# Kernel optimization log

Hardware: AMD Instinct MI355X
Metric: run time of the kernel (lower is better)

## Reference

```python
import jax, jax.numpy as jnp
import numpy as np

NEG_BIG = -1e12
ALPHA = 0.2  # LeakyReLU negative slope

def setup_inputs() -> dict:
    key = jax.random.key(0)
    k1, k2, k3, k4, k5 = jax.random.split(key, 5)
    N, F_in, F_out = 8192, 256, 128
    inp = jax.random.normal(k1, (N, F_in), dtype=jnp.float32)
    adj = jax.random.randint(k2, (N, N), 0, 2, dtype=jnp.int32)
    W = jax.random.normal(k3, (F_in, F_out), dtype=jnp.float32) * 0.05
    W_2 = jax.random.normal(k4, (F_in, F_out), dtype=jnp.float32) * 0.05
    W_3 = jax.random.normal(k5, (F_in, F_out), dtype=jnp.float32) * 0.05
    return {"inp": inp, "adj": adj, "W": W, "W_2": W_2, "W_3": W_3}

def reference(inp, adj, W, W_2, W_3):
    # h = inp @ W, h_2 = inp @ W_2  -> scores e = LeakyReLU(h @ h_2^T)  [N, N]
    h = inp @ W
    h_2 = inp @ W_2
    e = jax.nn.leaky_relu(h @ h_2.T, negative_slope=ALPHA)
    # adjacency mask, row softmax (dropout disabled: eval mode)
    attention = jax.nn.softmax(jnp.where(adj > 0, e, NEG_BIG), axis=1)
    h_3 = inp @ W_3
    h_prime = attention @ h_3
    return jax.nn.elu(h_prime)  # concat=True path
```

## Files before the change

### kernel.cpp

```cpp
#include <hip/hip_runtime.h>
#include <hip/hip_fp16.h>

#define N    8192
#define FIN  256
#define FOUT 128
#define BM   64
#define BN   64

typedef _Float16 half8 __attribute__((ext_vector_type(8)));
typedef _Float16 half4v __attribute__((ext_vector_type(4)));
typedef float floatx4 __attribute__((ext_vector_type(4)));

__global__ __launch_bounds__(256)
void maskprep_kernel(const int* __restrict__ adj,
                     unsigned long long* __restrict__ Msk)
{
    const int tid  = threadIdx.x;
    const int wave = tid >> 6;
    const int lane = tid & 63;
    const int task = blockIdx.x * 4 + wave;
    const int row  = task >> 3;
    const int g0   = (task & 7) * 4;
    const int4* base = (const int4*)(adj + (size_t)row * N);
    int4 v[4];
#pragma unroll
    for (int gg = 0; gg < 4; gg++) v[gg] = base[(g0 + gg) * 64 + lane];
#pragma unroll
    for (int gg = 0; gg < 4; gg++) {
        unsigned long long b0 = __ballot(v[gg].x != 0);
        unsigned long long b1 = __ballot(v[gg].y != 0);
        unsigned long long b2 = __ballot(v[gg].z != 0);
        unsigned long long b3 = __ballot(v[gg].w != 0);
        if (lane == 0) {
            unsigned long long* p = &Msk[((size_t)row * 32 + g0 + gg) * 4];
            *(ulonglong2*)&p[0] = make_ulonglong2(b0, b1);
            *(ulonglong2*)&p[2] = make_ulonglong2(b2, b3);
        }
    }
}

__global__ __launch_bounds__(256)
void wprep_kernel(const float* __restrict__ W0,
                  const float* __restrict__ W1,
                  const float* __restrict__ W2,
                  _Float16* __restrict__ Wf)
{
    int idx  = blockIdx.x * 256 + threadIdx.x;
    int lane = idx & 63;
    int frag = idx >> 6;
    int w    = frag >> 6;
    int f    = frag & 63;
    int nt   = f >> 3, kc = f & 7;
    int quad = lane >> 4, lo16 = lane & 15;
    const float* Wp = w == 0 ? W0 : (w == 1 ? W1 : W2);
    half8 v;
#pragma unroll
    for (int jj = 0; jj < 8; jj++)
        v[jj] = (_Float16)Wp[(size_t)(kc * 32 + quad * 8 + jj) * FOUT + nt * 16 + lo16];
    *(half8*)&Wf[(size_t)idx * 8] = v;
}

__global__ __launch_bounds__(256, 2)
void gemm3_kernel(const float* __restrict__ inp,
                  const _Float16* __restrict__ Wf,
                  _Float16* __restrict__ H,
                  _Float16* __restrict__ H2,
                  _Float16* __restrict__ H3T)
{
    const int which = blockIdx.z;
    const int c0    = blockIdx.y * 64;
    const _Float16* Wfw = Wf + (size_t)which * 64 * 64 * 8;
    const int r0 = blockIdx.x * 64;
    const int tid  = threadIdx.x;
    const int wave = tid >> 6;
    const int lane = tid & 63;
    const int lo16 = lane & 15;
    const int quad = lane >> 4;
    const int r = r0 + wave * 16 + lo16;

    half8 a[8];
#pragma unroll
    for (int kc = 0; kc < 8; kc++) {
        const float* p = &inp[(size_t)r * FIN + kc * 32 + quad * 8];
        float4 v0 = *(const float4*)p;
        float4 v1 = *(const float4*)(p + 4);
        a[kc][0] = (_Float16)v0.x; a[kc][1] = (_Float16)v0.y;
        a[kc][2] = (_Float16)v0.z; a[kc][3] = (_Float16)v0.w;
        a[kc][4] = (_Float16)v1.x; a[kc][5] = (_Float16)v1.y;
        a[kc][6] = (_Float16)v1.z; a[kc][7] = (_Float16)v1.w;
    }

    floatx4 acc[4];
#pragma unroll
    for (int i = 0; i < 4; i++) acc[i] = (floatx4){0.f, 0.f, 0.f, 0.f};

#pragma unroll
    for (int kc = 0; kc < 8; kc++)
#pragma unroll
        for (int nt = 0; nt < 4; nt++) {
            int ntg = (c0 >> 4) + nt;
            half8 b = *(const half8*)&Wfw[(((size_t)ntg * 8 + kc) * 64 + lane) * 8];
            acc[nt] = __builtin_amdgcn_mfma_f32_16x16x32_f16(a[kc], b, acc[nt], 0, 0, 0);
        }

    const int arow = wave * 16 + quad * 4;
    if (which < 2) {
        _Float16* outp = which == 0 ? H : H2;
#pragma unroll
        for (int nt = 0; nt < 4; nt++)
#pragma unroll
            for (int rr = 0; rr < 4; rr++)
                outp[(size_t)(r0 + arow + rr) * FOUT + c0 + nt * 16 + lo16] = (_Float16)acc[nt][rr];
    } else {
#pragma unroll
        for (int nt = 0; nt < 4; nt++) {
            half4v v;
#pragma unroll
            for (int rr = 0; rr < 4; rr++) v[rr] = (_Float16)acc[nt][rr];
            *(half4v*)&H3T[(size_t)(c0 + nt * 16 + lo16) * N + r0 + arow] = v;
        }
    }
}

__global__ __launch_bounds__(256)
void repackK_kernel(const _Float16* __restrict__ H2, _Float16* __restrict__ Kf)
{
    int idx  = blockIdx.x * 256 + threadIdx.x;
    int lane = idx & 63;
    int frag = idx >> 6;
    int jb = frag >> 4, f = frag & 15, nt = f >> 2, kc = f & 3;
    int quad = lane >> 4, lo16 = lane & 15;
    half8 v = *(const half8*)&H2[(size_t)(jb * 64 + nt * 16 + lo16) * FOUT + kc * 32 + quad * 8];
    *(half8*)&Kf[(size_t)idx * 8] = v;
}

__global__ __launch_bounds__(256)
void repackV_kernel(const _Float16* __restrict__ H3T, _Float16* __restrict__ Vf)
{
    int idx  = blockIdx.x * 256 + threadIdx.x;
    int lane = idx & 63;
    int frag = idx >> 6;
    int jb = frag >> 4, f = frag & 15, nt = f >> 1, kc = f & 1;
    int quad = lane >> 4, lo16 = lane & 15;
    half8 v = *(const half8*)&H3T[(size_t)(nt * 16 + lo16) * N + jb * 64 + kc * 32 + quad * 8];
    *(half8*)&Vf[(size_t)idx * 8] = v;
}

template<int JS>
__global__ __launch_bounds__(256, 2)
void attn_kernel(const _Float16* __restrict__ Hq,
                 const _Float16* __restrict__ Kf,
                 const _Float16* __restrict__ Vf,
                 const unsigned long long* __restrict__ Msk,
                 float* __restrict__ Opart,
                 float* __restrict__ mpart,
                 float* __restrict__ lpart)
{
    __shared__ _Float16 Ps[4][16][BN + 8];

    const int tid  = threadIdx.x;
    const int wave = tid >> 6;
    const int lane = tid & 63;
    const int lo16 = lane & 15;
    const int quad = lane >> 4;
    const int bid  = blockIdx.x;
    const int js   = bid & (JS - 1);
    const int ib   = bid / JS;
    const int i0   = ib * BM;
    const int jbeg = js * (N / JS);
    const int e    = lo16 & 3;
    const int lsh  = lo16 >> 2;

    half8 q[4];
#pragma unroll
    for (int kc = 0; kc < 4; kc++)
        q[kc] = *(const half8*)&Hq[(size_t)(i0 + wave * 16 + lo16) * FOUT + kc * 32 + quad * 8];

    floatx4 O[8];
#pragma unroll
    for (int i = 0; i < 8; i++) O[i] = (floatx4){0.f, 0.f, 0.f, 0.f};
    float m_r[4], l_r[4];
#pragma unroll
    for (int r = 0; r < 4; r++) { m_r[r] = -1e12f; l_r[r] = 0.f; }

    const int arow = i0 + wave * 16 + quad * 4;

    for (int it = 0; it < (N / JS) / BN; it++) {
        const int j0 = jbeg + it * BN;
        const int jb = j0 >> 6;
        const int grp = (j0 >> 8) * 4;
        const int bofs = ((j0 & 255) >> 2) + lsh;

        const _Float16* kfp = Kf + (size_t)jb * 16 * 64 * 8;
        half8 kf[16];
#pragma unroll
        for (int f = 0; f < 16; f++)
            kf[f] = *(const half8*)&kfp[((size_t)f * 64 + lane) * 8];
        const _Float16* vfp = Vf + (size_t)jb * 16 * 64 * 8;
        half8 vf[16];
#pragma unroll
        for (int f = 0; f < 16; f++)
            vf[f] = *(const half8*)&vfp[((size_t)f * 64 + lane) * 8];
        unsigned long long mw[4];
#pragma unroll
        for (int r = 0; r < 4; r++)
            mw[r] = Msk[(size_t)(arow + r) * 128 + e + grp];

        floatx4 S[4];
#pragma unroll
        for (int nt = 0; nt < 4; nt++) {
            S[nt] = (floatx4){0.f, 0.f, 0.f, 0.f};
#pragma unroll
            for (int kc = 0; kc < 4; kc++)
                S[nt] = __builtin_amdgcn_mfma_f32_16x16x32_f16(q[kc], kf[nt * 4 + kc], S[nt], 0, 0, 0);
        }

        float sv[4][4];
#pragma unroll
        for (int nt = 0; nt < 4; nt++)
#pragma unroll
            for (int r = 0; r < 4; r++) {
                float ev = S[nt][r];
                ev = ev > 0.f ? ev : 0.2f * ev;
                sv[nt][r] = ((mw[r] >> (bofs + nt * 4)) & 1ull) ? ev : -1e12f;
            }

        float alpha[4];
#pragma unroll
        for (int r = 0; r < 4; r++) {
            float v = fmaxf(fmaxf(sv[0][r], sv[1][r]), fmaxf(sv[2][r], sv[3][r]));
#pragma unroll
            for (int d = 1; d < 16; d <<= 1)
                v = fmaxf(v, __shfl_xor(v, d));
            float mn = fmaxf(m_r[r], v);
            alpha[r] = __expf(m_r[r] - mn);
            m_r[r] = mn;
        }

        float rs[4] = {0.f, 0.f, 0.f, 0.f};
#pragma unroll
        for (int nt = 0; nt < 4; nt++)
#pragma unroll
            for (int r = 0; r < 4; r++) {
                float p = __expf(sv[nt][r] - m_r[r]);
                rs[r] += p;
                Ps[wave][quad * 4 + r][nt * 16 + lo16] = (_Float16)p;
            }
#pragma unroll
        for (int r = 0; r < 4; r++) {
            float v = rs[r];
#pragma unroll
            for (int d = 1; d < 16; d <<= 1)
                v += __shfl_xor(v, d);
            l_r[r] = l_r[r] * alpha[r] + v;
#pragma unroll
            for (int nt = 0; nt < 8; nt++)
                O[nt][r] *= alpha[r];
        }

        asm volatile("s_waitcnt lgkmcnt(0)" ::: "memory");

#pragma unroll
        for (int kc = 0; kc < BN / 32; kc++) {
            half8 pa = *(const half8*)&Ps[wave][lo16][kc * 32 + quad * 8];
#pragma unroll
            for (int nt = 0; nt < 8; nt++)
                O[nt] = __builtin_amdgcn_mfma_f32_16x16x32_f16(pa, vf[nt * 2 + kc], O[nt], 0, 0, 0);
        }
    }

#pragma unroll
    for (int nt = 0; nt < 8; nt++)
#pragma unroll
        for (int r = 0; r < 4; r++)
            Opart[((size_t)js * N + arow + r) * FOUT + nt * 16 + lo16] = O[nt][r];
    if (lo16 == 0) {
#pragma unroll
        for (int r = 0; r < 4; r++) {
            mpart[js * N + arow + r] = m_r[r];
            lpart[js * N + arow + r] = l_r[r];
        }
    }
}

template<int JS>
__global__ __launch_bounds__(256)
void combine_kernel(const float* __restrict__ Opart,
                    const float* __restrict__ mpart,
                    const float* __restrict__ lpart,
                    float* __restrict__ out)
{
    int idx = blockIdx.x * 256 + threadIdx.x;
    int i = idx >> 5;
    int c = (idx & 31) << 2;
    float m[JS];
    float M = -3.0e38f;
#pragma unroll
    for (int s = 0; s < JS; s++) { m[s] = mpart[s * N + i]; M = fmaxf(M, m[s]); }
    float w[JS];
    float L = 0.f;
#pragma unroll
    for (int s = 0; s < JS; s++) { w[s] = __expf(m[s] - M); L += lpart[s * N + i] * w[s]; }
    float4 o = {0.f, 0.f, 0.f, 0.f};
#pragma unroll
    for (int s = 0; s < JS; s++) {
        float4 v = *(const float4*)&Opart[((size_t)s * N + i) * FOUT + c];
        o.x += w[s] * v.x; o.y += w[s] * v.y; o.z += w[s] * v.z; o.w += w[s] * v.w;
    }
    float inv = 1.f / L;
    float r0 = o.x * inv, r1 = o.y * inv, r2 = o.z * inv, r3 = o.w * inv;
    float4 res;
    res.x = r0 > 0.f ? r0 : __expf(r0) - 1.f;
    res.y = r1 > 0.f ? r1 : __expf(r1) - 1.f;
    res.z = r2 > 0.f ? r2 : __expf(r2) - 1.f;
    res.w = r3 > 0.f ? r3 : __expf(r3) - 1.f;
    *(float4*)&out[(size_t)i * FOUT + c] = res;
}

extern "C" void kernel_launch(void* const* d_in, const int* in_sizes, int n_in,
                              void* d_out, int out_size, void* d_ws, size_t ws_size,
                              hipStream_t stream) {
    const float* inp = (const float*)d_in[0];
    const int*   adj = (const int*)d_in[1];
    const float* W0  = (const float*)d_in[2];
    const float* W1  = (const float*)d_in[3];
    const float* W2  = (const float*)d_in[4];
    float* out = (float*)d_out;

    char* ws = (char*)d_ws;
    _Float16* H   = (_Float16*)(ws);
    _Float16* H2  = (_Float16*)(ws + (2u << 20));
    _Float16* H3T = (_Float16*)(ws + (4u << 20));
    _Float16* Wf  = (_Float16*)(ws + (6u << 20));
    unsigned long long* Msk = (unsigned long long*)(ws + (7u << 20));
    _Float16* Kf  = (_Float16*)(ws + (15u << 20));
    _Float16* Vf  = (_Float16*)(ws + (17u << 20));
    float* Opart  = (float*)(ws + (19u << 20));

    const size_t need8 = (19ull << 20) + 8ull * N * FOUT * 4 + 2ull * 8 * N * 4;

    maskprep_kernel<<<16384, 256, 0, stream>>>(adj, Msk);
    wprep_kernel<<<48, 256, 0, stream>>>(W0, W1, W2, Wf);
    gemm3_kernel<<<dim3(N / 64, 2, 3), 256, 0, stream>>>(inp, Wf, H, H2, H3T);
    repackK_kernel<<<512, 256, 0, stream>>>(H2, Kf);
    repackV_kernel<<<512, 256, 0, stream>>>(H3T, Vf);

    if (ws_size >= need8) {
        constexpr int JS = 8;
        float* mpart = (float*)(ws + (19u << 20) + (size_t)JS * N * FOUT * 4);
        float* lpart = mpart + (size_t)JS * N;
        attn_kernel<JS><<<(N / BM) * JS, 256, 0, stream>>>(H, Kf, Vf, Msk, Opart, mpart, lpart);
        combine_kernel<JS><<<(N * FOUT / 4) / 256, 256, 0, stream>>>(Opart, mpart, lpart, out);
    } else {
        constexpr int JS = 4;
        float* mpart = (float*)(ws + (19u << 20) + (size_t)JS * N * FOUT * 4);
        float* lpart = mpart + (size_t)JS * N;
        attn_kernel<JS><<<(N / BM) * JS, 256, 0, stream>>>(H, Kf, Vf, Msk, Opart, mpart, lpart);
        combine_kernel<JS><<<(N * FOUT / 4) / 256, 256, 0, stream>>>(Opart, mpart, lpart, out);
    }
}
```

Baseline: 480.7 us.

## Stage K/V tiles through double-buffered LDS shared across waves

Previously each of the four waves loaded the same K and V fragments from global memory into registers. Now the block loads each K/V tile once into a double-buffered LDS array, prefetching the next tile into registers while computing on the current one. This cuts redundant global and L2 traffic fourfold and overlaps loads with MFMA work. In exchange it uses 64KB of LDS per block, which may limit occupancy under launch_bounds(256,2), and adds a __syncthreads per iteration.

```diff
diff --git a/kernel.cpp b/kernel.cpp
--- a/kernel.cpp
+++ b/kernel.cpp
@@ -156,6 +156,7 @@
                  float* __restrict__ mpart,
                  float* __restrict__ lpart)
 {
+    __shared__ _Float16 KV[2][16384];
     __shared__ _Float16 Ps[4][16][BN + 8];
 
     const int tid  = threadIdx.x;
@@ -170,6 +171,7 @@
     const int jbeg = js * (N / JS);
     const int e    = lo16 & 3;
     const int lsh  = lo16 >> 2;
+    const int NIT  = (N / JS) / BN;
 
     half8 q[4];
 #pragma unroll
@@ -184,35 +186,55 @@
     for (int r = 0; r < 4; r++) { m_r[r] = -1e12f; l_r[r] = 0.f; }
 
     const int arow = i0 + wave * 16 + quad * 4;
-
-    for (int it = 0; it < (N / JS) / BN; it++) {
+    const int soff = ((size_t)0, (tid * 8));
+
+    {
+        const int jb0 = jbeg >> 6;
+        const _Float16* gk = Kf + (size_t)jb0 * 8192;
+        const _Float16* gv = Vf + (size_t)jb0 * 8192;
+#pragma unroll
+        for (int r = 0; r < 4; r++) {
+            int off = (r * 256 + tid) * 8;
+            *(half8*)&KV[0][off]        = *(const half8*)&gk[off];
+            *(half8*)&KV[0][8192 + off] = *(const half8*)&gv[off];
+        }
+        __syncthreads();
+    }
+
+    int cur = 0;
+    for (int it = 0; it < NIT; it++) {
         const int j0 = jbeg + it * BN;
-        const int jb = j0 >> 6;
         const int grp = (j0 >> 8) * 4;
         const int bofs = ((j0 & 255) >> 2) + lsh;
 
-        const _Float16* kfp = Kf + (size_t)jb * 16 * 64 * 8;
-        half8 kf[16];
-#pragma unroll
-        for (int f = 0; f < 16; f++)
-            kf[f] = *(const half8*)&kfp[((size_t)f * 64 + lane) * 8];
-        const _Float16* vfp = Vf + (size_t)jb * 16 * 64 * 8;
-        half8 vf[16];
-#pragma unroll
-        for (int f = 0; f < 16; f++)
-            vf[f] = *(const half8*)&vfp[((size_t)f * 64 + lane) * 8];
+        half8 st[8];
+        if (it + 1 < NIT) {
+            const int jbn = (j0 + BN) >> 6;
+            const _Float16* gk = Kf + (size_t)jbn * 8192;
+            const _Float16* gv = Vf + (size_t)jbn * 8192;
+#pragma unroll
+            for (int r = 0; r < 4; r++) {
+                int off = (r * 256 + tid) * 8;
+                st[r]     = *(const half8*)&gk[off];
+                st[r + 4] = *(const half8*)&gv[off];
+            }
+        }
         unsigned long long mw[4];
 #pragma unroll
         for (int r = 0; r < 4; r++)
             mw[r] = Msk[(size_t)(arow + r) * 128 + e + grp];
 
+        const _Float16* kb = &KV[cur][0];
+        const _Float16* vb = &KV[cur][8192];
         floatx4 S[4];
 #pragma unroll
         for (int nt = 0; nt < 4; nt++) {
             S[nt] = (floatx4){0.f, 0.f, 0.f, 0.f};
 #pragma unroll
-            for (int kc = 0; kc < 4; kc++)
-                S[nt] = __builtin_amdgcn_mfma_f32_16x16x32_f16(q[kc], kf[nt * 4 + kc], S[nt], 0, 0, 0);
+            for (int kc = 0; kc < 4; kc++) {
+                half8 b = *(const half8*)&kb[((nt * 4 + kc) * 64 + lane) * 8];
+                S[nt] = __builtin_amdgcn_mfma_f32_16x16x32_f16(q[kc], b, S[nt], 0, 0, 0);
+            }
         }
 
         float sv[4][4];
@@ -264,9 +286,23 @@
         for (int kc = 0; kc < BN / 32; kc++) {
             half8 pa = *(const half8*)&Ps[wave][lo16][kc * 32 + quad * 8];
 #pragma unroll
-            for (int nt = 0; nt < 8; nt++)
-                O[nt] = __builtin_amdgcn_mfma_f32_16x16x32_f16(pa, vf[nt * 2 + kc], O[nt], 0, 0, 0);
-        }
+            for (int nt = 0; nt < 8; nt++) {
+                half8 b = *(const half8*)&vb[((nt * 2 + kc) * 64 + lane) * 8];
+                O[nt] = __builtin_amdgcn_mfma_f32_16x16x32_f16(pa, b, O[nt], 0, 0, 0);
+            }
+        }
+
+        if (it + 1 < NIT) {
+            const int nxt = cur ^ 1;
+#pragma unroll
+            for (int r = 0; r < 4; r++) {
+                int off = (r * 256 + tid) * 8;
+                *(half8*)&KV[nxt][off]        = st[r];
+                *(half8*)&KV[nxt][8192 + off] = st[r + 4];
+            }
+        }
+        __syncthreads();
+        cur ^= 1;
     }
 
 #pragma unroll
```

New measurement: 477.9 us. Within noise of the previous version (-0.6%).
